# Kernel tuning notes

Hardware: AMD Instinct MI355X
Metric: run time of the kernel (lower is better)

The kernel has to match this reference:

```python
import jax, jax.numpy as jnp
import numpy as np
from jax import lax

DN = ('NCDHW', 'OIDHW', 'NCDHW')


def dwconv(x, w, b):
    # depthwise 3D conv, 'same' padding (groups == channels of this branch)
    k = w.shape[-1]
    p = k // 2
    y = lax.conv_general_dilated(x, w, (1, 1, 1), [(p, p)] * 3,
                                 dimension_numbers=DN,
                                 feature_group_count=x.shape[1])
    return y + b[None, :, None, None, None]


def group_norm(x, w, b, groups=4, eps=1e-5):
    B, C, D, H, W = x.shape
    xr = x.reshape(B, groups, C // groups, D, H, W)
    mu = xr.mean(axis=(2, 3, 4, 5), keepdims=True)
    var = xr.var(axis=(2, 3, 4, 5), keepdims=True)
    xn = ((xr - mu) / jnp.sqrt(var + eps)).reshape(B, C, D, H, W)
    return xn * w[None, :, None, None, None] + b[None, :, None, None, None]


def instance_norm(x, eps=1e-5):
    # torch InstanceNorm3d default: affine=False, biased var, per (n,c) over spatial
    mu = x.mean(axis=(2, 3, 4), keepdims=True)
    var = x.var(axis=(2, 3, 4), keepdims=True)
    return (x - mu) / jnp.sqrt(var + eps)


def setup_inputs() -> dict:
    key = jax.random.key(0)
    B, C, D, H, W = 2, 32, 64, 64, 64
    gc = C // 4
    keys = jax.random.split(key, 12)
    inp = {"x": jax.random.normal(keys[0], (B, C, D, H, W), jnp.float32)}
    for i, k in enumerate([3, 5, 7, 9]):
        inp[f"w{k}"] = jax.random.normal(keys[1 + i], (gc, 1, k, k, k), jnp.float32) * (1.0 / k ** 1.5)
        inp[f"b{k}"] = jax.random.normal(keys[5 + i], (gc,), jnp.float32) * 0.01
    inp["gn_w"] = jnp.ones((C,), jnp.float32)
    inp["gn_b"] = jnp.zeros((C,), jnp.float32)
    inp["w_pw"] = jax.random.normal(keys[9], (gc, C), jnp.float32) * (1.0 / np.sqrt(C))
    inp["w_nxn"] = jax.random.normal(keys[10], (C, gc, 3, 3, 3), jnp.float32) * (1.0 / np.sqrt(gc * 27))
    return inp


def reference(x, w3, b3, w5, b5, w7, b7, w9, b9, gn_w, gn_b, w_pw, w_nxn):
    # split into 4 channel groups -> multi-kernel depthwise conv branches
    l, gs, gm, gl = jnp.split(x, 4, axis=1)
    y = jnp.concatenate([dwconv(l, w3, b3), dwconv(gs, w5, b5),
                         dwconv(gm, w7, b7), dwconv(gl, w9, b9)], axis=1) + x
    # GroupNorm(4) + exact GELU
    y = jax.nn.gelu(group_norm(y, gn_w, gn_b), approximate=False)
    # 1x1x1 conv (bias=False) + InstanceNorm + SiLU
    y = jax.nn.silu(instance_norm(jnp.einsum('bcdhw,oc->bodhw', y, w_pw)))
    # 3x3x3 conv (bias=False, pad 1) + InstanceNorm + SiLU
    y = lax.conv_general_dilated(y, w_nxn, (1, 1, 1), [(1, 1)] * 3, dimension_numbers=DN)
    y = jax.nn.silu(instance_norm(y))
    return y + x
```

## Files before the change

kernel.cpp:

```cpp
#include <hip/hip_runtime.h>
#include <cstddef>

#define SPATIAL (64*64*64)


__device__ __forceinline__ float wave_reduce(float v) {
    #pragma unroll
    for (int off = 32; off; off >>= 1) v += __shfl_down(v, off);
    return v;
}

__global__ void zero_stats(float* __restrict__ stats) {
    if (threadIdx.x < 176) stats[threadIdx.x] = 0.0f;
}


__device__ __forceinline__ void dw_stage(const float* __restrict__ xin,
                                         float* __restrict__ ring, int zd, int h0) {
    float* dst = ring + ((zd + 36) % 9) * 1728;
    const float* src = xin + ((size_t)zd << 12);
    const bool dok = (unsigned)zd < 64u;
    for (int i = threadIdx.x; i < 1728; i += 256) {
        const int row = i / 72;
        const int col = i - row * 72;
        const int zh = h0 - 4 + row;
        const int zw = col - 4;
        float v = 0.0f;
        if (dok & ((unsigned)zh < 64u) & ((unsigned)zw < 64u)) v = src[(zh << 6) + zw];
        dst[i] = v;
    }
}

template<int K>
__device__ __forceinline__ void dw_impl(const float* __restrict__ x,
                                        const float* __restrict__ wsrc, float bias,
                                        int bc, int h0, int d0,
                                        float* __restrict__ ring,
                                        float* __restrict__ stats, int b,
                                        float* __restrict__ y1)
{
    constexpr int P = K / 2;
    constexpr int G = P - 1;
    const float* xin = x + ((size_t)bc << 18);

    for (int zd = d0 - P; zd < d0 + P; ++zd) dw_stage(xin, ring, zd, h0);

    const int r  = threadIdx.x >> 4;
    const int w0 = (threadIdx.x & 15) << 2;
    float gsum = 0.0f, gsq = 0.0f;

    for (int d = d0; d < d0 + 16; ++d) {
        dw_stage(xin, ring, d + P, h0);
        __syncthreads();

        float a0 = bias, a1 = bias, a2 = bias, a3 = bias;
        for (int kd = 0; kd < K; ++kd) {
            const float* sl = ring + ((d + kd - P + 36) % 9) * 1728;
            const float* wrow0 = wsrc + kd * K * K;
            #pragma unroll
            for (int kh = 0; kh < K; ++kh) {
                const float* rowp = sl + (r + kh + (4 - P)) * 72 + w0;
                const float4 A  = *(const float4*)rowp;
                const float4 B4 = *(const float4*)(rowp + 4);
                const float4 C4 = *(const float4*)(rowp + 8);
                const float win[12] = {A.x,A.y,A.z,A.w, B4.x,B4.y,B4.z,B4.w,
                                       C4.x,C4.y,C4.z,C4.w};
                const float* wr = wrow0 + kh * K;
                #pragma unroll
                for (int kw = 0; kw < K; ++kw) {
                    const float wt = wr[kw];
                    a0 += win[kw + 4 - P] * wt;
                    a1 += win[kw + 5 - P] * wt;
                    a2 += win[kw + 6 - P] * wt;
                    a3 += win[kw + 7 - P] * wt;
                }
            }
        }
        const float* cen = ring + ((d + 36) % 9) * 1728 + (r + 4) * 72 + (w0 + 4);
        const float4 xc = *(const float4*)cen;
        a0 += xc.x; a1 += xc.y; a2 += xc.z; a3 += xc.w;

        *(float4*)(y1 + ((size_t)bc << 18) + ((size_t)d << 12) +
                   ((size_t)(h0 + r) << 6) + w0) = make_float4(a0, a1, a2, a3);
        gsum += a0 + a1 + a2 + a3;
        gsq  += a0*a0 + a1*a1 + a2*a2 + a3*a3;
        __syncthreads();
    }

    gsum = wave_reduce(gsum);
    gsq  = wave_reduce(gsq);
    if ((threadIdx.x & 63) == 0) {
        atomicAdd(&stats[b * 4 + G], gsum);
        atomicAdd(&stats[8 + b * 4 + G], gsq);
    }
}

__global__ __launch_bounds__(256) void dwconv_kernel(
    const float* __restrict__ x,
    const float* __restrict__ w3, const float* __restrict__ b3,
    const float* __restrict__ w5, const float* __restrict__ b5,
    const float* __restrict__ w7, const float* __restrict__ b7,
    const float* __restrict__ w9, const float* __restrict__ b9,
    float* __restrict__ y1, float* __restrict__ stats)
{
    __shared__ float ring[9 * 1728];
    const int gid = blockIdx.x;
    const int g   = 3 - (gid >> 8);
    const int rr  = gid & 255;
    const int plane = rr >> 4;
    const int hq  = (rr >> 2) & 3;
    const int dc  = rr & 3;
    const int b   = plane >> 3, cl = plane & 7;
    const int bc  = (b << 5) + (g << 3) + cl;
    const int h0  = hq << 4, d0 = dc << 4;

    switch (g) {
        case 0: dw_impl<3>(x, w3 + cl * 27,  b3[cl], bc, h0, d0, ring, stats, b, y1); break;
        case 1: dw_impl<5>(x, w5 + cl * 125, b5[cl], bc, h0, d0, ring, stats, b, y1); break;
        case 2: dw_impl<7>(x, w7 + cl * 343, b7[cl], bc, h0, d0, ring, stats, b, y1); break;
        default: dw_impl<9>(x, w9 + cl * 729, b9[cl], bc, h0, d0, ring, stats, b, y1); break;
    }
}

__global__ void gn_finalize(const float* __restrict__ gn_w, const float* __restrict__ gn_b,
                            float* __restrict__ stats)
{
    const int i = threadIdx.x;
    if (i >= 64) return;
    const int b = i >> 5, c = i & 31, g = c >> 3;
    const float N = 8.0f * (float)SPATIAL;
    const float mu  = stats[b * 4 + g] / N;
    const float var = stats[8 + b * 4 + g] / N - mu * mu;
    const float rs  = rsqrtf(var + 1e-5f);
    const float a   = gn_w[c] * rs;
    stats[176 + i] = a;
    stats[240 + i] = gn_b[c] - mu * a;
}

__global__ __launch_bounds__(256) void pw_kernel(
    const float* __restrict__ y1, const float* __restrict__ w_pw,
    float* __restrict__ t, float* __restrict__ stats)
{
    const int bid = blockIdx.x;
    const int b   = bid >> 8;
    const int s0  = ((bid & 255) * 256 + threadIdx.x) * 4;
    const int s   = (bid & 255) * 1024 + threadIdx.x * 4;
    (void)s0;

    const float* yb = y1 + ((size_t)b << 23);
    float acc[8][4] = {};

    for (int c = 0; c < 32; ++c) {
        const float ga = stats[176 + b * 32 + c];
        const float gs = stats[240 + b * 32 + c];
        const float4 y = *(const float4*)(yb + ((size_t)c << 18) + s);
        float v0 = ga * y.x + gs, v1 = ga * y.y + gs, v2 = ga * y.z + gs, v3 = ga * y.w + gs;
        const float e0 = 0.5f * v0 * (1.0f + erff(v0 * 0.70710678118654752f));
        const float e1 = 0.5f * v1 * (1.0f + erff(v1 * 0.70710678118654752f));
        const float e2 = 0.5f * v2 * (1.0f + erff(v2 * 0.70710678118654752f));
        const float e3 = 0.5f * v3 * (1.0f + erff(v3 * 0.70710678118654752f));
        #pragma unroll
        for (int o = 0; o < 8; ++o) {
            const float wt = w_pw[o * 32 + c];
            acc[o][0] += e0 * wt; acc[o][1] += e1 * wt;
            acc[o][2] += e2 * wt; acc[o][3] += e3 * wt;
        }
    }

    float* tb = t + ((size_t)b << 21);
    #pragma unroll
    for (int o = 0; o < 8; ++o) {
        *(float4*)(tb + ((size_t)o << 18) + s) =
            make_float4(acc[o][0], acc[o][1], acc[o][2], acc[o][3]);
        float sm = acc[o][0] + acc[o][1] + acc[o][2] + acc[o][3];
        float sq = acc[o][0]*acc[o][0] + acc[o][1]*acc[o][1] +
                   acc[o][2]*acc[o][2] + acc[o][3]*acc[o][3];
        sm = wave_reduce(sm);
        sq = wave_reduce(sq);
        if ((threadIdx.x & 63) == 0) {
            atomicAdd(&stats[16 + b * 8 + o], sm);
            atomicAdd(&stats[32 + b * 8 + o], sq);
        }
    }
}

__global__ void in2_finalize(float* __restrict__ stats)
{
    const int i = threadIdx.x;
    if (i >= 16) return;
    const float N = (float)SPATIAL;
    const float mu  = stats[16 + i] / N;
    const float var = stats[32 + i] / N - mu * mu;
    stats[304 + i] = mu;
    stats[320 + i] = rsqrtf(var + 1e-5f);
}

__device__ __forceinline__ void c3_stage(const float* __restrict__ tb,
                                         float* __restrict__ ls,
                                         const float* __restrict__ stats,
                                         int b, int zd, int h0, int w0g)
{
    const bool dok = (unsigned)zd < 64u;
    const int slot = (zd + 33) % 3;
    for (int i = threadIdx.x; i < 3200; i += 256) {
        const int c   = i / 400;
        const int rem = i - c * 400;
        const int row = rem / 40;
        const int col = rem - row * 40;
        const int zh  = h0 - 1 + row;
        const int zw  = w0g + col - 4;
        float v = 0.0f;
        if (dok & ((unsigned)zh < 64u) & ((unsigned)zw < 64u)) {
            const float raw = tb[((size_t)c << 18) + ((size_t)zd << 12) + (zh << 6) + zw];
            const float mu = stats[304 + (b << 3) + c];
            const float rs = stats[320 + (b << 3) + c];
            const float xn = (raw - mu) * rs;
            v = xn / (1.0f + expf(-xn));
        }
        ls[c * 1200 + slot * 400 + row * 40 + col] = v;
    }
}

__global__ __launch_bounds__(256) void conv3_kernel(
    const float* __restrict__ t, const float* __restrict__ w_nxn,
    float* __restrict__ out, float* __restrict__ stats)
{
    __shared__ float ls[9600];
    const int bid = blockIdx.x;
    const int b   = bid >> 7;
    const int r7  = bid & 127;
    const int d0  = (r7 >> 4) << 3;
    const int h0  = ((r7 >> 1) & 7) << 3;
    const int w0g = (r7 & 1) << 5;

    const int tid = threadIdx.x;
    const int w0  = (tid & 7) << 2;
    const int r   = (tid >> 3) & 7;
    const int oq  = __builtin_amdgcn_readfirstlane(tid >> 6);
    const int o0  = oq << 3;

    const float* tb = t + ((size_t)b << 21);
    float s3[8] = {}, q3[8] = {};

    c3_stage(tb, ls, stats, b, d0 - 1, h0, w0g);
    c3_stage(tb, ls, stats, b, d0,     h0, w0g);

    for (int d = d0; d < d0 + 8; ++d) {
        c3_stage(tb, ls, stats, b, d + 1, h0, w0g);
        __syncthreads();

        float acc[8][4] = {};
        for (int c = 0; c < 8; ++c) {
            const float* lc = ls + c * 1200;
            const float* wc = w_nxn + c * 27;
            #pragma unroll
            for (int kd = 0; kd < 3; ++kd) {
                const float* sl = lc + ((d + kd + 32) % 3) * 400;
                #pragma unroll
                for (int kh = 0; kh < 3; ++kh) {
                    const float* rowp = sl + (r + kh) * 40 + w0;
                    const float4 A  = *(const float4*)rowp;
                    const float4 B4 = *(const float4*)(rowp + 4);
                    const float4 C4 = *(const float4*)(rowp + 8);
                    const float win[12] = {A.x,A.y,A.z,A.w, B4.x,B4.y,B4.z,B4.w,
                                           C4.x,C4.y,C4.z,C4.w};
                    #pragma unroll
                    for (int oi = 0; oi < 8; ++oi) {
                        const float* wp = wc + (o0 + oi) * 216 + kd * 9 + kh * 3;
                        #pragma unroll
                        for (int kw = 0; kw < 3; ++kw) {
                            const float wt = wp[kw];
                            acc[oi][0] += win[kw + 3] * wt;
                            acc[oi][1] += win[kw + 4] * wt;
                            acc[oi][2] += win[kw + 5] * wt;
                            acc[oi][3] += win[kw + 6] * wt;
                        }
                    }
                }
            }
        }

        #pragma unroll
        for (int oi = 0; oi < 8; ++oi) {
            const int o = o0 + oi;
            *(float4*)(out + ((size_t)((b << 5) + o) << 18) + ((size_t)d << 12) +
                       ((size_t)(h0 + r) << 6) + (w0g + w0)) =
                make_float4(acc[oi][0], acc[oi][1], acc[oi][2], acc[oi][3]);
            s3[oi] += acc[oi][0] + acc[oi][1] + acc[oi][2] + acc[oi][3];
            q3[oi] += acc[oi][0]*acc[oi][0] + acc[oi][1]*acc[oi][1] +
                      acc[oi][2]*acc[oi][2] + acc[oi][3]*acc[oi][3];
        }
        __syncthreads();
    }

    #pragma unroll
    for (int oi = 0; oi < 8; ++oi) {
        float sm = wave_reduce(s3[oi]);
        float sq = wave_reduce(q3[oi]);
        if ((tid & 63) == 0) {
            atomicAdd(&stats[48 + (b << 5) + o0 + oi], sm);
            atomicAdd(&stats[112 + (b << 5) + o0 + oi], sq);
        }
    }
}

__global__ void in3_finalize(float* __restrict__ stats)
{
    const int i = threadIdx.x;
    if (i >= 64) return;
    const float N = (float)SPATIAL;
    const float mu  = stats[48 + i] / N;
    const float var = stats[112 + i] / N - mu * mu;
    stats[336 + i] = mu;
    stats[400 + i] = rsqrtf(var + 1e-5f);
}

__global__ __launch_bounds__(256) void final_kernel(
    const float* __restrict__ x, float* __restrict__ out, const float* __restrict__ stats)
{
    const int idx = blockIdx.x * 256 + threadIdx.x;
    const size_t i4 = (size_t)idx << 2;
    const int bc = (int)(i4 >> 18);
    const float mu = stats[336 + bc], rs = stats[400 + bc];
    float4 v = *(const float4*)(out + i4);
    const float4 xr = *(const float4*)(x + i4);
    v.x = (v.x - mu) * rs; v.x = v.x / (1.0f + expf(-v.x)) + xr.x;
    v.y = (v.y - mu) * rs; v.y = v.y / (1.0f + expf(-v.y)) + xr.y;
    v.z = (v.z - mu) * rs; v.z = v.z / (1.0f + expf(-v.z)) + xr.z;
    v.w = (v.w - mu) * rs; v.w = v.w / (1.0f + expf(-v.w)) + xr.w;
    *(float4*)(out + i4) = v;
}

extern "C" void kernel_launch(void* const* d_in, const int* in_sizes, int n_in,
                              void* d_out, int out_size, void* d_ws, size_t ws_size,
                              hipStream_t stream)
{
    const float* x    = (const float*)d_in[0];
    const float* w3   = (const float*)d_in[1];
    const float* b3   = (const float*)d_in[2];
    const float* w5   = (const float*)d_in[3];
    const float* b5   = (const float*)d_in[4];
    const float* w7   = (const float*)d_in[5];
    const float* b7   = (const float*)d_in[6];
    const float* w9   = (const float*)d_in[7];
    const float* b9   = (const float*)d_in[8];
    const float* gn_w = (const float*)d_in[9];
    const float* gn_b = (const float*)d_in[10];
    const float* w_pw = (const float*)d_in[11];
    const float* w_nxn= (const float*)d_in[12];

    char* ws = (char*)d_ws;
    float* t     = (float*)ws;
    float* stats = (float*)(ws + 16777216);

    float* out = (float*)d_out;

    zero_stats<<<1, 256, 0, stream>>>(stats);
    dwconv_kernel<<<1024, 256, 0, stream>>>(x, w3, b3, w5, b5, w7, b7, w9, b9, out, stats);
    gn_finalize<<<1, 64, 0, stream>>>(gn_w, gn_b, stats);
    pw_kernel<<<512, 256, 0, stream>>>(out, w_pw, t, stats);
    in2_finalize<<<1, 16, 0, stream>>>(stats);
    conv3_kernel<<<256, 256, 0, stream>>>(t, w_nxn, out, stats);
    in3_finalize<<<1, 64, 0, stream>>>(stats);
    final_kernel<<<16384, 256, 0, stream>>>(x, out, stats);
}
```

Before: 1.218 ms.

## Retile depthwise and 3x3x3 conv kernels with padded LDS strides and more blocks

The depthwise conv now gives each thread 8 outputs along W, with each wave handling a different depth slice of a 4-slice group. It uses a 12-slice LDS ring with a 73-float row stride to avoid bank conflicts, and halves the H tile so twice as many blocks launch. The 3x3x3 conv uses a 41-float padded row stride, loads only a 6-wide window per row, and halves the depth tile to double the grid. The pointwise kernel batches 8 channel loads ahead of the GELU math to expose memory-level parallelism. The trade-offs are more halo restaging per block and scalar LDS loads in place of float4 loads.

Measured after the change: 1.035 ms. -15.0%, faster.

```diff
diff --git a/kernel.cpp b/kernel.cpp
--- a/kernel.cpp
+++ b/kernel.cpp
@@ -15,14 +15,18 @@
 }
 
 
+#define DW_RS   73
+#define DW_SLICE (16 * DW_RS)
+#define DW_RING 12
+
 __device__ __forceinline__ void dw_stage(const float* __restrict__ xin,
                                          float* __restrict__ ring, int zd, int h0) {
-    float* dst = ring + ((zd + 36) % 9) * 1728;
+    float* dst = ring + ((zd + 24) % DW_RING) * DW_SLICE;
     const float* src = xin + ((size_t)zd << 12);
     const bool dok = (unsigned)zd < 64u;
-    for (int i = threadIdx.x; i < 1728; i += 256) {
-        const int row = i / 72;
-        const int col = i - row * 72;
+    for (int i = threadIdx.x; i < DW_SLICE; i += 256) {
+        const int row = i / DW_RS;
+        const int col = i - row * DW_RS;
         const int zh = h0 - 4 + row;
         const int zw = col - 4;
         float v = 0.0f;
@@ -41,49 +45,55 @@
 {
     constexpr int P = K / 2;
     constexpr int G = P - 1;
+    constexpr int WIN = 8 + 2 * P;
     const float* xin = x + ((size_t)bc << 18);
 
     for (int zd = d0 - P; zd < d0 + P; ++zd) dw_stage(xin, ring, zd, h0);
 
-    const int r  = threadIdx.x >> 4;
-    const int w0 = (threadIdx.x & 15) << 2;
+    const int lane = threadIdx.x & 63;
+    const int wave = threadIdx.x >> 6;
+    const int w0   = (lane & 7) << 3;
+    const int r    = lane >> 3;
     float gsum = 0.0f, gsq = 0.0f;
 
-    for (int d = d0; d < d0 + 16; ++d) {
-        dw_stage(xin, ring, d + P, h0);
+    for (int dq = d0; dq < d0 + 16; dq += 4) {
+        #pragma unroll
+        for (int j = 0; j < 4; ++j) dw_stage(xin, ring, dq + P + j, h0);
         __syncthreads();
 
-        float a0 = bias, a1 = bias, a2 = bias, a3 = bias;
+        const int dd = dq + wave;
+        float acc[8];
+        #pragma unroll
+        for (int i = 0; i < 8; ++i) acc[i] = bias;
+
         for (int kd = 0; kd < K; ++kd) {
-            const float* sl = ring + ((d + kd - P + 36) % 9) * 1728;
-            const float* wrow0 = wsrc + kd * K * K;
+            const float* sl = ring + ((dd + kd - P + 24) % DW_RING) * DW_SLICE;
+            const float* wk = wsrc + kd * K * K;
             #pragma unroll
             for (int kh = 0; kh < K; ++kh) {
-                const float* rowp = sl + (r + kh + (4 - P)) * 72 + w0;
-                const float4 A  = *(const float4*)rowp;
-                const float4 B4 = *(const float4*)(rowp + 4);
-                const float4 C4 = *(const float4*)(rowp + 8);
-                const float win[12] = {A.x,A.y,A.z,A.w, B4.x,B4.y,B4.z,B4.w,
-                                       C4.x,C4.y,C4.z,C4.w};
-                const float* wr = wrow0 + kh * K;
+                const float* rowp = sl + (r + kh + 4 - P) * DW_RS + (w0 + 4 - P);
+                float win[WIN];
+                #pragma unroll
+                for (int j = 0; j < WIN; ++j) win[j] = rowp[j];
+                const float* wr = wk + kh * K;
                 #pragma unroll
                 for (int kw = 0; kw < K; ++kw) {
                     const float wt = wr[kw];
-                    a0 += win[kw + 4 - P] * wt;
-                    a1 += win[kw + 5 - P] * wt;
-                    a2 += win[kw + 6 - P] * wt;
-                    a3 += win[kw + 7 - P] * wt;
+                    #pragma unroll
+                    for (int i = 0; i < 8; ++i) acc[i] += win[kw + i] * wt;
                 }
             }
         }
-        const float* cen = ring + ((d + 36) % 9) * 1728 + (r + 4) * 72 + (w0 + 4);
-        const float4 xc = *(const float4*)cen;
-        a0 += xc.x; a1 += xc.y; a2 += xc.z; a3 += xc.w;
-
-        *(float4*)(y1 + ((size_t)bc << 18) + ((size_t)d << 12) +
-                   ((size_t)(h0 + r) << 6) + w0) = make_float4(a0, a1, a2, a3);
-        gsum += a0 + a1 + a2 + a3;
-        gsq  += a0*a0 + a1*a1 + a2*a2 + a3*a3;
+        const float* cen = ring + ((dd + 24) % DW_RING) * DW_SLICE + (r + 4) * DW_RS + (w0 + 4);
+        #pragma unroll
+        for (int i = 0; i < 8; ++i) acc[i] += cen[i];
+
+        const size_t base = ((size_t)bc << 18) + ((size_t)dd << 12) +
+                            ((size_t)(h0 + r) << 6) + w0;
+        *(float4*)(y1 + base)     = make_float4(acc[0], acc[1], acc[2], acc[3]);
+        *(float4*)(y1 + base + 4) = make_float4(acc[4], acc[5], acc[6], acc[7]);
+        #pragma unroll
+        for (int i = 0; i < 8; ++i) { gsum += acc[i]; gsq += acc[i] * acc[i]; }
         __syncthreads();
     }
 
@@ -103,16 +113,16 @@
     const float* __restrict__ w9, const float* __restrict__ b9,
     float* __restrict__ y1, float* __restrict__ stats)
 {
-    __shared__ float ring[9 * 1728];
+    __shared__ float ring[DW_RING * DW_SLICE];
     const int gid = blockIdx.x;
-    const int g   = 3 - (gid >> 8);
-    const int rr  = gid & 255;
-    const int plane = rr >> 4;
-    const int hq  = (rr >> 2) & 3;
+    const int g   = 3 - (gid >> 9);
+    const int rr  = gid & 511;
+    const int plane = rr >> 5;
+    const int hq  = (rr >> 2) & 7;
     const int dc  = rr & 3;
     const int b   = plane >> 3, cl = plane & 7;
     const int bc  = (b << 5) + (g << 3) + cl;
-    const int h0  = hq << 4, d0 = dc << 4;
+    const int h0  = hq << 3, d0 = dc << 4;
 
     switch (g) {
         case 0: dw_impl<3>(x, w3 + cl * 27,  b3[cl], bc, h0, d0, ring, stats, b, y1); break;
@@ -143,27 +153,33 @@
 {
     const int bid = blockIdx.x;
     const int b   = bid >> 8;
-    const int s0  = ((bid & 255) * 256 + threadIdx.x) * 4;
     const int s   = (bid & 255) * 1024 + threadIdx.x * 4;
-    (void)s0;
 
     const float* yb = y1 + ((size_t)b << 23);
     float acc[8][4] = {};
 
-    for (int c = 0; c < 32; ++c) {
-        const float ga = stats[176 + b * 32 + c];
-        const float gs = stats[240 + b * 32 + c];
-        const float4 y = *(const float4*)(yb + ((size_t)c << 18) + s);
-        float v0 = ga * y.x + gs, v1 = ga * y.y + gs, v2 = ga * y.z + gs, v3 = ga * y.w + gs;
-        const float e0 = 0.5f * v0 * (1.0f + erff(v0 * 0.70710678118654752f));
-        const float e1 = 0.5f * v1 * (1.0f + erff(v1 * 0.70710678118654752f));
-        const float e2 = 0.5f * v2 * (1.0f + erff(v2 * 0.70710678118654752f));
-        const float e3 = 0.5f * v3 * (1.0f + erff(v3 * 0.70710678118654752f));
-        #pragma unroll
-        for (int o = 0; o < 8; ++o) {
-            const float wt = w_pw[o * 32 + c];
-            acc[o][0] += e0 * wt; acc[o][1] += e1 * wt;
-            acc[o][2] += e2 * wt; acc[o][3] += e3 * wt;
+    for (int cc = 0; cc < 32; cc += 8) {
+        float4 yv[8];
+        #pragma unroll
+        for (int u = 0; u < 8; ++u)
+            yv[u] = *(const float4*)(yb + ((size_t)(cc + u) << 18) + s);
+        #pragma unroll
+        for (int u = 0; u < 8; ++u) {
+            const int c = cc + u;
+            const float ga = stats[176 + b * 32 + c];
+            const float gs = stats[240 + b * 32 + c];
+            float v0 = ga * yv[u].x + gs, v1 = ga * yv[u].y + gs;
+            float v2 = ga * yv[u].z + gs, v3 = ga * yv[u].w + gs;
+            const float e0 = 0.5f * v0 * (1.0f + erff(v0 * 0.70710678118654752f));
+            const float e1 = 0.5f * v1 * (1.0f + erff(v1 * 0.70710678118654752f));
+            const float e2 = 0.5f * v2 * (1.0f + erff(v2 * 0.70710678118654752f));
+            const float e3 = 0.5f * v3 * (1.0f + erff(v3 * 0.70710678118654752f));
+            #pragma unroll
+            for (int o = 0; o < 8; ++o) {
+                const float wt = w_pw[o * 32 + c];
+                acc[o][0] += e0 * wt; acc[o][1] += e1 * wt;
+                acc[o][2] += e2 * wt; acc[o][3] += e3 * wt;
+            }
         }
     }
 
@@ -195,6 +211,10 @@
     stats[320 + i] = rsqrtf(var + 1e-5f);
 }
 
+#define C3_RS 41
+#define C3_ROWSZ (10 * C3_RS)
+#define C3_CH (3 * C3_ROWSZ)
+
 __device__ __forceinline__ void c3_stage(const float* __restrict__ tb,
                                          float* __restrict__ ls,
                                          const float* __restrict__ stats,
@@ -202,11 +222,11 @@
 {
     const bool dok = (unsigned)zd < 64u;
     const int slot = (zd + 33) % 3;
-    for (int i = threadIdx.x; i < 3200; i += 256) {
-        const int c   = i / 400;
-        const int rem = i - c * 400;
-        const int row = rem / 40;
-        const int col = rem - row * 40;
+    for (int i = threadIdx.x; i < 8 * C3_ROWSZ; i += 256) {
+        const int c   = i / C3_ROWSZ;
+        const int rem = i - c * C3_ROWSZ;
+        const int row = rem / C3_RS;
+        const int col = rem - row * C3_RS;
         const int zh  = h0 - 1 + row;
         const int zw  = w0g + col - 4;
         float v = 0.0f;
@@ -217,7 +237,7 @@
             const float xn = (raw - mu) * rs;
             v = xn / (1.0f + expf(-xn));
         }
-        ls[c * 1200 + slot * 400 + row * 40 + col] = v;
+        ls[c * C3_CH + slot * C3_ROWSZ + row * C3_RS + col] = v;
     }
 }
 
@@ -225,13 +245,13 @@
     const float* __restrict__ t, const float* __restrict__ w_nxn,
     float* __restrict__ out, float* __restrict__ stats)
 {
-    __shared__ float ls[9600];
+    __shared__ float ls[8 * C3_CH];
     const int bid = blockIdx.x;
-    const int b   = bid >> 7;
-    const int r7  = bid & 127;
-    const int d0  = (r7 >> 4) << 3;
-    const int h0  = ((r7 >> 1) & 7) << 3;
-    const int w0g = (r7 & 1) << 5;
+    const int b   = bid >> 8;
+    const int r8  = bid & 255;
+    const int d0  = (r8 >> 4) << 2;
+    const int h0  = ((r8 >> 1) & 7) << 3;
+    const int w0g = (r8 & 1) << 5;
 
     const int tid = threadIdx.x;
     const int w0  = (tid & 7) << 2;
@@ -245,35 +265,33 @@
     c3_stage(tb, ls, stats, b, d0 - 1, h0, w0g);
     c3_stage(tb, ls, stats, b, d0,     h0, w0g);
 
-    for (int d = d0; d < d0 + 8; ++d) {
+    for (int d = d0; d < d0 + 4; ++d) {
         c3_stage(tb, ls, stats, b, d + 1, h0, w0g);
         __syncthreads();
 
         float acc[8][4] = {};
         for (int c = 0; c < 8; ++c) {
-            const float* lc = ls + c * 1200;
+            const float* lc = ls + c * C3_CH;
             const float* wc = w_nxn + c * 27;
             #pragma unroll
             for (int kd = 0; kd < 3; ++kd) {
-                const float* sl = lc + ((d + kd + 32) % 3) * 400;
+                const float* sl = lc + ((d + kd + 32) % 3) * C3_ROWSZ;
                 #pragma unroll
                 for (int kh = 0; kh < 3; ++kh) {
-                    const float* rowp = sl + (r + kh) * 40 + w0;
-                    const float4 A  = *(const float4*)rowp;
-                    const float4 B4 = *(const float4*)(rowp + 4);
-                    const float4 C4 = *(const float4*)(rowp + 8);
-                    const float win[12] = {A.x,A.y,A.z,A.w, B4.x,B4.y,B4.z,B4.w,
-                                           C4.x,C4.y,C4.z,C4.w};
+                    const float* rowp = sl + (r + kh) * C3_RS + w0 + 3;
+                    float win[6];
+                    #pragma unroll
+                    for (int j = 0; j < 6; ++j) win[j] = rowp[j];
                     #pragma unroll
                     for (int oi = 0; oi < 8; ++oi) {
                         const float* wp = wc + (o0 + oi) * 216 + kd * 9 + kh * 3;
                         #pragma unroll
                         for (int kw = 0; kw < 3; ++kw) {
                             const float wt = wp[kw];
-                            acc[oi][0] += win[kw + 3] * wt;
-                            acc[oi][1] += win[kw + 4] * wt;
-                            acc[oi][2] += win[kw + 5] * wt;
-                            acc[oi][3] += win[kw + 6] * wt;
+                            acc[oi][0] += win[kw]     * wt;
+                            acc[oi][1] += win[kw + 1] * wt;
+                            acc[oi][2] += win[kw + 2] * wt;
+                            acc[oi][3] += win[kw + 3] * wt;
                         }
                     }
                 }
@@ -356,11 +374,11 @@
     float* out = (float*)d_out;
 
     zero_stats<<<1, 256, 0, stream>>>(stats);
-    dwconv_kernel<<<1024, 256, 0, stream>>>(x, w3, b3, w5, b5, w7, b7, w9, b9, out, stats);
+    dwconv_kernel<<<2048, 256, 0, stream>>>(x, w3, b3, w5, b5, w7, b7, w9, b9, out, stats);
     gn_finalize<<<1, 64, 0, stream>>>(gn_w, gn_b, stats);
     pw_kernel<<<512, 256, 0, stream>>>(out, w_pw, t, stats);
     in2_finalize<<<1, 16, 0, stream>>>(stats);
-    conv3_kernel<<<256, 256, 0, stream>>>(t, w_nxn, out, stats);
+    conv3_kernel<<<512, 256, 0, stream>>>(t, w_nxn, out, stats);
     in3_finalize<<<1, 64, 0, stream>>>(stats);
     final_kernel<<<16384, 256, 0, stream>>>(x, out, stats);
 }
```
